# Optimization experiments

Hardware: AMD Instinct MI355X
Metric: run time of the kernel (lower is better)

Reference implementation:

```python
import jax, jax.numpy as jnp
import numpy as np

EPS = 1e-5

def _layernorm(x, g, b):
    mu = jnp.mean(x, axis=-1, keepdims=True)
    var = jnp.mean(jnp.square(x - mu), axis=-1, keepdims=True)
    return (x - mu) * jax.lax.rsqrt(var + EPS) * g + b

def setup_inputs() -> dict:
    key = jax.random.key(0)
    B, N, C, MID = 1, 512, 128, 128
    ks = jax.random.split(key, 12)
    s_c = 1.0 / np.sqrt(C)
    s_m = 1.0 / np.sqrt(MID)
    return {
        "act": jax.random.normal(ks[0], (B, N, N, C), dtype=jnp.float32),
        "mask": jnp.ones((B, N, N), dtype=jnp.float32),
        # input LayerNorm
        "ln_in_g": jnp.ones((C,), jnp.float32),
        "ln_in_b": jnp.zeros((C,), jnp.float32),
        # left/right projections and gates (Linear: y = x @ W + b)
        "wl": jax.random.normal(ks[1], (C, MID), jnp.float32) * s_c,
        "bl": jnp.zeros((MID,), jnp.float32),
        "wr": jax.random.normal(ks[2], (C, MID), jnp.float32) * s_c,
        "br": jnp.zeros((MID,), jnp.float32),
        "wgl": jax.random.normal(ks[3], (C, MID), jnp.float32) * s_c,
        "bgl": jnp.zeros((MID,), jnp.float32),
        "wgr": jax.random.normal(ks[4], (C, MID), jnp.float32) * s_c,
        "bgr": jnp.zeros((MID,), jnp.float32),
        # output gating linear (C -> C)
        "wgate": jax.random.normal(ks[5], (C, C), jnp.float32) * s_c,
        "bgate": jnp.zeros((C,), jnp.float32),
        # center LayerNorm (over MID)
        "ln_c_g": jnp.ones((MID,), jnp.float32),
        "ln_c_b": jnp.zeros((MID,), jnp.float32),
        # output projection (MID -> C)
        "wout": jax.random.normal(ks[6], (MID, C), jnp.float32) * s_m,
        "bout": jnp.zeros((C,), jnp.float32),
    }

def reference(act, mask, ln_in_g, ln_in_b, wl, bl, wr, br, wgl, bgl, wgr, bgr,
              wgate, bgate, ln_c_g, ln_c_b, wout, bout):
    x = _layernorm(act, ln_in_g, ln_in_b)          # [B,N,N,C]
    m = mask[..., None]                             # [B,N,N,1]
    left_proj = m * (x @ wl + bl) * jax.nn.sigmoid(x @ wgl + bgl)   # [B,N,N,MID]
    right_proj = m * (x @ wr + br) * jax.nn.sigmoid(x @ wgr + bgr)  # [B,N,N,MID]
    gate_values = x @ wgate + bgate                 # [B,N,N,C]
    # triangle outgoing: contract over k (second index of both)
    out = jnp.einsum('bikc,bjkc->bijc', left_proj, right_proj)      # [B,N,N,MID]
    out = _layernorm(out, ln_c_g, ln_c_b)
    out = out @ wout + bout                         # [B,N,N,C]
    return out * jax.nn.sigmoid(gate_values)
```

## Files before the change

kernel.cpp:

```cpp
#include <hip/hip_runtime.h>

#define NPOS 512
#define NN_ (512 * 512)

typedef unsigned short u16;
typedef __attribute__((ext_vector_type(8))) short bf16x8_t;
typedef __attribute__((ext_vector_type(4))) float f32x4_t;

__device__ __forceinline__ float bf2f(u16 u) {
  union { unsigned int i; float f; } v;
  v.i = ((unsigned int)u) << 16;
  return v.f;
}
__device__ __forceinline__ u16 f2bf(float f) {
  __bf16 h = (__bf16)f;
  return __builtin_bit_cast(unsigned short, h);
}
__device__ __forceinline__ float sigm(float x) { return 1.0f / (1.0f + __expf(-x)); }

__device__ __forceinline__ void gld_lds16(u16* lds, const u16* g) {
  __builtin_amdgcn_global_load_lds(
      (const __attribute__((address_space(1))) unsigned int*)g,
      (__attribute__((address_space(3))) unsigned int*)lds, 16, 0, 0);
}

__global__ __launch_bounds__(256) void k0_wt(const float* __restrict__ wl,
                                             const float* __restrict__ wgl,
                                             const float* __restrict__ wr,
                                             const float* __restrict__ wgr,
                                             const float* __restrict__ wgate,
                                             u16* __restrict__ wtbase) {
  int b = blockIdx.x;
  int wi = b >> 3;
  int o0 = (b & 7) * 16;
  const float* W = wi == 0 ? wl : wi == 1 ? wgl : wi == 2 ? wr : wi == 3 ? wgr : wgate;
  u16* dst = wtbase + wi * 16384;
  int t = threadIdx.x;
  int o = o0 + (t >> 4);
  int k0 = (t & 15) * 8;
  float v[8];
#pragma unroll
  for (int i = 0; i < 8; ++i) v[i] = W[(k0 + i) * 128 + o];
  ushort4 a, b4;
  a.x = f2bf(v[0]); a.y = f2bf(v[1]); a.z = f2bf(v[2]); a.w = f2bf(v[3]);
  b4.x = f2bf(v[4]); b4.y = f2bf(v[5]); b4.z = f2bf(v[6]); b4.w = f2bf(v[7]);
  *(ushort4*)(dst + o * 128 + k0) = a;
  *(ushort4*)(dst + o * 128 + k0 + 4) = b4;
}

__global__ __launch_bounds__(256) void k0b(const float* __restrict__ wout,
                                           u16* __restrict__ Wt6) {
  int o = blockIdx.x * 16 + (threadIdx.x >> 4);
  int k0 = (threadIdx.x & 15) * 8;
  float v[8];
#pragma unroll
  for (int i = 0; i < 8; ++i) v[i] = wout[(k0 + i) * 128 + o];
  ushort4 a, b4;
  a.x = f2bf(v[0]); a.y = f2bf(v[1]); a.z = f2bf(v[2]); a.w = f2bf(v[3]);
  b4.x = f2bf(v[4]); b4.y = f2bf(v[5]); b4.z = f2bf(v[6]); b4.w = f2bf(v[7]);
  *(ushort4*)(Wt6 + o * 128 + k0) = a;
  *(ushort4*)(Wt6 + o * 128 + k0 + 4) = b4;
}

__global__ __launch_bounds__(512, 4) void k2_fused(
    const float* __restrict__ act, const float* __restrict__ mask,
    const u16* __restrict__ wtbase,
    const float* __restrict__ ln_g, const float* __restrict__ ln_b,
    const float* __restrict__ bl, const float* __restrict__ bgl,
    const float* __restrict__ br, const float* __restrict__ bgr,
    const float* __restrict__ bgate,
    u16* __restrict__ Lt, u16* __restrict__ Rt, u16* __restrict__ Gs) {
  __shared__ __align__(16) unsigned char smem[81920];
  u16* xn  = (u16*)smem;
  u16* wh0 = (u16*)(smem + 32768);
  u16* wh1 = (u16*)(smem + 49152);
  u16* ob  = (u16*)(smem + 65536);

  int tid = threadIdx.x;
  int l = tid & 63, w = tid >> 6;
  int wr_ = w >> 1, wc = w & 1;
  int lr = l & 15, lk = l >> 4;
  size_t p0 = (size_t)blockIdx.x * 128;

#define STAGE(i_, buf_)                                                     \
  {                                                                         \
    const u16* src = wtbase + ((i_) >> 1) * 16384 + ((i_) & 1) * 8192;      \
    _Pragma("unroll") for (int q = 0; q < 2; ++q) {                         \
      int s = q * 512 + tid;                                                \
      int row = s >> 4, j = (s & 15) ^ (row & 7);                           \
      gld_lds16((buf_) + s * 8, src + row * 128 + j * 8);                   \
    }                                                                       \
  }
#define ZERO(ACC)                                                           \
  { ACC[0][0] = (f32x4_t){0.f, 0.f, 0.f, 0.f};                              \
    ACC[0][1] = (f32x4_t){0.f, 0.f, 0.f, 0.f};                              \
    ACC[1][0] = (f32x4_t){0.f, 0.f, 0.f, 0.f};                              \
    ACC[1][1] = (f32x4_t){0.f, 0.f, 0.f, 0.f}; }
#define MFK(buf_, ACC, KT, AF0, AF1)                                        \
  {                                                                         \
    int kb = (KT) * 4 + lk;                                                 \
    int o0_ = wc * 32 + lr, o1_ = wc * 32 + 16 + lr;                        \
    bf16x8_t bfr0 = *(const bf16x8_t*)((buf_) + o0_ * 128 + ((kb ^ (o0_ & 7)) * 8)); \
    bf16x8_t bfr1 = *(const bf16x8_t*)((buf_) + o1_ * 128 + ((kb ^ (o1_ & 7)) * 8)); \
    ACC[0][0] = __builtin_amdgcn_mfma_f32_16x16x32_bf16(AF0, bfr0, ACC[0][0], 0, 0, 0); \
    ACC[0][1] = __builtin_amdgcn_mfma_f32_16x16x32_bf16(AF0, bfr1, ACC[0][1], 0, 0, 0); \
    ACC[1][0] = __builtin_amdgcn_mfma_f32_16x16x32_bf16(AF1, bfr0, ACC[1][0], 0, 0, 0); \
    ACC[1][1] = __builtin_amdgcn_mfma_f32_16x16x32_bf16(AF1, bfr1, ACC[1][1], 0, 0, 0); \
  }
#define MF(buf_, ACC)                                                       \
  MFK(buf_, ACC, 0, af00, af10)                                             \
  MFK(buf_, ACC, 1, af01, af11)                                             \
  MFK(buf_, ACC, 2, af02, af12)                                             \
  MFK(buf_, ACC, 3, af03, af13)
#define MFPAIR(ACCP, ACCG)                                                  \
  __builtin_amdgcn_s_setprio(1);                                            \
  ZERO(ACCP); MF(wh0, ACCP);                                                \
  ZERO(ACCG); MF(wh1, ACCG);                                                \
  __builtin_amdgcn_s_setprio(0);
#define EPW(ACCP, ACCG, Bp_, Bg_, obase_)                                   \
  {                                                                         \
    float bpv[2], bgv[2];                                                   \
    _Pragma("unroll") for (int n = 0; n < 2; ++n) {                         \
      int og = (obase_) + wc * 32 + n * 16 + lr;                            \
      bpv[n] = Bp_[og]; bgv[n] = Bg_[og];                                   \
    }                                                                       \
    _Pragma("unroll") for (int m = 0; m < 2; ++m) {                         \
      int p4 = wr_ * 32 + m * 16 + lk * 4;                                  \
      float4 mk = *(const float4*)(mask + p0 + p4);                         \
      int slot = p4 >> 3, off = p4 & 7;                                     \
      _Pragma("unroll") for (int n = 0; n < 2; ++n) {                       \
        int ol = wc * 32 + n * 16 + lr;                                     \
        ushort4 v;                                                          \
        v.x = f2bf(mk.x * (ACCP[m][n][0] + bpv[n]) * sigm(ACCG[m][n][0] + bgv[n])); \
        v.y = f2bf(mk.y * (ACCP[m][n][1] + bpv[n]) * sigm(ACCG[m][n][1] + bgv[n])); \
        v.z = f2bf(mk.z * (ACCP[m][n][2] + bpv[n]) * sigm(ACCG[m][n][2] + bgv[n])); \
        v.w = f2bf(mk.w * (ACCP[m][n][3] + bpv[n]) * sigm(ACCG[m][n][3] + bgv[n])); \
        *(ushort4*)(ob + ol * 128 + ((slot ^ (ol & 7)) << 3) + off) = v;    \
      }                                                                     \
    }                                                                       \
  }
#define GEPW(ACC, obase_)                                                   \
  {                                                                         \
    float bgv[2];                                                           \
    _Pragma("unroll") for (int n = 0; n < 2; ++n)                           \
      bgv[n] = bgate[(obase_) + wc * 32 + n * 16 + lr];                     \
    _Pragma("unroll") for (int m = 0; m < 2; ++m) {                         \
      int p4 = wr_ * 32 + m * 16 + lk * 4;                                  \
      int slot = p4 >> 3, off = p4 & 7;                                     \
      _Pragma("unroll") for (int n = 0; n < 2; ++n) {                       \
        int ol = wc * 32 + n * 16 + lr;                                     \
        ushort4 v;                                                          \
        v.x = f2bf(ACC[m][n][0] + bgv[n]);                                  \
        v.y = f2bf(ACC[m][n][1] + bgv[n]);                                  \
        v.z = f2bf(ACC[m][n][2] + bgv[n]);                                  \
        v.w = f2bf(ACC[m][n][3] + bgv[n]);                                  \
        *(ushort4*)(ob + ol * 128 + ((slot ^ (ol & 7)) << 3) + off) = v;    \
      }                                                                     \
    }                                                                       \
  }
#define EPS(Tdst_, obase_)                                                  \
  {                                                                         \
    _Pragma("unroll") for (int it = 0; it < 2; ++it) {                      \
      int s = it * 512 + tid;                                               \
      int ol = s >> 4, c8 = s & 15;                                         \
      *(uint4*)(Tdst_ + (size_t)((obase_) + ol) * NN_ + p0 + c8 * 8) =      \
          *(const uint4*)(ob + ol * 128 + ((c8 ^ (ol & 7)) << 3));          \
    }                                                                       \
  }

  STAGE(0, wh0);
  STAGE(2, wh1);

#pragma unroll
  for (int r = 0; r < 8; ++r) {
    int f = r * 512 + tid;
    int pos = f >> 5, c4 = f & 31;
    float4 v = *(const float4*)(act + (p0 + pos) * 128 + c4 * 4);
    float s1 = v.x + v.y + v.z + v.w;
    float s2 = v.x * v.x + v.y * v.y + v.z * v.z + v.w * v.w;
#pragma unroll
    for (int m = 1; m < 32; m <<= 1) {
      s1 += __shfl_xor(s1, m);
      s2 += __shfl_xor(s2, m);
    }
    float mu = s1 * (1.0f / 128.0f);
    float rstd = rsqrtf(s2 * (1.0f / 128.0f) - mu * mu + 1e-5f);
    int cb = c4 * 4;
    float4 gg = *(const float4*)(ln_g + cb);
    float4 bb = *(const float4*)(ln_b + cb);
    ushort4 o4;
    o4.x = f2bf((v.x - mu) * rstd * gg.x + bb.x);
    o4.y = f2bf((v.y - mu) * rstd * gg.y + bb.y);
    o4.z = f2bf((v.z - mu) * rstd * gg.z + bb.z);
    o4.w = f2bf((v.w - mu) * rstd * gg.w + bb.w);
    int c8 = c4 >> 1, off = (c4 & 1) * 4;
    *(ushort4*)(xn + pos * 128 + ((c8 ^ (pos & 7)) << 3) + off) = o4;
  }
  __syncthreads();

  bf16x8_t af00, af01, af02, af03, af10, af11, af12, af13;
  {
    int row0 = wr_ * 32 + lr;
    int row1 = wr_ * 32 + 16 + lr;
    const u16* x0 = xn + row0 * 128;
    const u16* x1 = xn + row1 * 128;
    af00 = *(const bf16x8_t*)(x0 + (((0 * 4 + lk) ^ (row0 & 7)) * 8));
    af01 = *(const bf16x8_t*)(x0 + (((1 * 4 + lk) ^ (row0 & 7)) * 8));
    af02 = *(const bf16x8_t*)(x0 + (((2 * 4 + lk) ^ (row0 & 7)) * 8));
    af03 = *(const bf16x8_t*)(x0 + (((3 * 4 + lk) ^ (row0 & 7)) * 8));
    af10 = *(const bf16x8_t*)(x1 + (((0 * 4 + lk) ^ (row1 & 7)) * 8));
    af11 = *(const bf16x8_t*)(x1 + (((1 * 4 + lk) ^ (row1 & 7)) * 8));
    af12 = *(const bf16x8_t*)(x1 + (((2 * 4 + lk) ^ (row1 & 7)) * 8));
    af13 = *(const bf16x8_t*)(x1 + (((3 * 4 + lk) ^ (row1 & 7)) * 8));
  }

  f32x4_t ap[2][2], ag[2][2];

  MFPAIR(ap, ag);
  __syncthreads();
  STAGE(1, wh0);
  STAGE(3, wh1);
  EPW(ap, ag, bl, bgl, 0);
  __syncthreads();
  EPS(Lt, 0);

  MFPAIR(ap, ag);
  __syncthreads();
  STAGE(4, wh0);
  STAGE(6, wh1);
  EPW(ap, ag, bl, bgl, 64);
  __syncthreads();
  EPS(Lt, 64);

  MFPAIR(ap, ag);
  __syncthreads();
  STAGE(5, wh0);
  STAGE(7, wh1);
  EPW(ap, ag, br, bgr, 0);
  __syncthreads();
  EPS(Rt, 0);

  MFPAIR(ap, ag);
  __syncthreads();
  STAGE(8, wh0);
  STAGE(9, wh1);
  EPW(ap, ag, br, bgr, 64);
  __syncthreads();
  EPS(Rt, 64);

  MFPAIR(ap, ag);
  __syncthreads();
  GEPW(ap, 0);
  __syncthreads();
  EPS(Gs, 0);
  __syncthreads();
  GEPW(ag, 64);
  __syncthreads();
  EPS(Gs, 64);
#undef STAGE
#undef ZERO
#undef MFK
#undef MF
#undef MFPAIR
#undef EPW
#undef GEPW
#undef EPS
}

__global__ __launch_bounds__(256, 4) void k3_einsum_mfma(const u16* __restrict__ Lt,
                                                         const u16* __restrict__ Rt,
                                                         u16* __restrict__ Ot) {
  __shared__ __align__(16) u16 smem[2 * 128 * 64];
  u16* La = smem;
  u16* Rb = smem + 128 * 64;

  int tid = threadIdx.x;
  int bid = blockIdx.x;
  int swz = (bid & 7) * 256 + (bid >> 3);
  int c = swz >> 4;
  int t = swz & 15;
  int i0 = (t >> 2) << 7, j0 = (t & 3) << 7;
  const u16* Lg = Lt + (size_t)c * NN_ + (size_t)i0 * 512;
  const u16* Rg = Rt + (size_t)c * NN_ + (size_t)j0 * 512;

  int l = tid & 63, w = tid >> 6;
  int wr = w >> 1, wc = w & 1;
  int lr = l & 15, lk = l >> 4;

  f32x4_t acc[4][4];
#pragma unroll
  for (int m = 0; m < 4; ++m)
#pragma unroll
    for (int n = 0; n < 4; ++n) acc[m][n] = (f32x4_t){0.f, 0.f, 0.f, 0.f};

  for (int kt = 0; kt < 512; kt += 64) {
#pragma unroll
    for (int q = 0; q < 4; ++q) {
      int s = q * 256 + tid;
      int row = s >> 3;
      int k8 = (s & 7) ^ (row & 7);
      gld_lds16(La + s * 8, Lg + (size_t)row * 512 + kt + k8 * 8);
      gld_lds16(Rb + s * 8, Rg + (size_t)row * 512 + kt + k8 * 8);
    }
    __syncthreads();

    __builtin_amdgcn_s_setprio(1);
#pragma unroll
    for (int ks = 0; ks < 2; ++ks) {
      int kb = ks * 4 + lk;
      bf16x8_t af[4], bf[4];
#pragma unroll
      for (int m = 0; m < 4; ++m) {
        int row = wr * 64 + m * 16 + lr;
        af[m] = *(const bf16x8_t*)(La + row * 64 + ((kb ^ (row & 7)) * 8));
      }
#pragma unroll
      for (int n = 0; n < 4; ++n) {
        int row = wc * 64 + n * 16 + lr;
        bf[n] = *(const bf16x8_t*)(Rb + row * 64 + ((kb ^ (row & 7)) * 8));
      }
#pragma unroll
      for (int m = 0; m < 4; ++m)
#pragma unroll
        for (int n = 0; n < 4; ++n)
          acc[m][n] = __builtin_amdgcn_mfma_f32_16x16x32_bf16(af[m], bf[n], acc[m][n], 0, 0, 0);
    }
    __builtin_amdgcn_s_setprio(0);
    __syncthreads();
  }

  u16* ob = smem;
#pragma unroll
  for (int m = 0; m < 4; ++m) {
    int row0 = wr * 64 + m * 16 + lk * 4;
#pragma unroll
    for (int n = 0; n < 4; ++n) {
      int col = (wc * 64 + n * 16 + lr) ^ (lk << 4);
#pragma unroll
      for (int r = 0; r < 4; ++r)
        ob[(row0 + r) * 128 + col] = f2bf(acc[m][n][r]);
    }
  }
  __syncthreads();
#pragma unroll
  for (int it = 0; it < 8; ++it) {
    int s = it * 256 + tid;
    int row = s >> 4, c8 = s & 15;
    int g = (row >> 2) & 3;
    const u16* src = ob + row * 128 + ((c8 * 8) ^ (g << 4));
    *(uint4*)(Ot + (size_t)c * NN_ + (size_t)(i0 + row) * 512 + j0 + c8 * 8) =
        *(const uint4*)src;
  }
}

__global__ __launch_bounds__(512, 4) void k4_mfma(const u16* __restrict__ Ot,
                                                  const u16* __restrict__ Gs,
                                                  const u16* __restrict__ Wt6,
                                                  const float* __restrict__ gc,
                                                  const float* __restrict__ bc,
                                                  const float* __restrict__ bout,
                                                  float* __restrict__ out) {
  __shared__ __align__(16) unsigned char smem[70656];
  u16* ot = (u16*)smem;
  u16* ws = (u16*)(smem + 32768);
  float* ps = (float*)(smem + 65536);
  float* pss = (float*)(smem + 67584);
  float2* munr = (float2*)(smem + 69632);

  int tid = threadIdx.x;
  int l = tid & 63, w = tid >> 6;
  int wr = w >> 1, wc = w & 1;
  int lr = l & 15, lk = l >> 4;
  size_t p0 = (size_t)blockIdx.x * 128;
  int i_row = (int)(p0 >> 9);
  int j0 = (int)(p0 & 511);

#pragma unroll
  for (int q = 0; q < 4; ++q) {
    int s = q * 512 + tid;
    int cc = s >> 4, j = s & 15;
    gld_lds16(ot + s * 8, Ot + (size_t)cc * NN_ + (size_t)i_row * 512 + j0 + j * 8);
  }
#pragma unroll
  for (int q = 0; q < 4; ++q) {
    int s = q * 512 + tid;
    int o = s >> 4, j = (s & 15) ^ (o & 7);
    gld_lds16(ws + s * 8, Wt6 + o * 128 + j * 8);
  }
  __syncthreads();

  int g = tid >> 7, pos = tid & 127;
  float vals[32];
  float s1 = 0.0f, s2 = 0.0f;
#pragma unroll
  for (int m = 0; m < 32; ++m) {
    float v = bf2f(ot[(g * 32 + m) * 128 + pos]);
    vals[m] = v;
    s1 += v;
    s2 += v * v;
  }
  ps[g * 128 + pos] = s1;
  pss[g * 128 + pos] = s2;
  __syncthreads();
  if (tid < 128) {
    float a = ps[tid] + ps[128 + tid] + ps[256 + tid] + ps[384 + tid];
    float b = pss[tid] + pss[128 + tid] + pss[256 + tid] + pss[384 + tid];
    float mu = a * (1.0f / 128.0f);
    float rstd = rsqrtf(b * (1.0f / 128.0f) - mu * mu + 1e-5f);
    munr[tid] = make_float2(mu, rstd);
  }
  __syncthreads();
  float2 mr = munr[pos];

  u16* xn = ot;
#pragma unroll
  for (int mm = 0; mm < 4; ++mm) {
    int c8 = g * 4 + mm;
    ushort4 va, vb;
    int cb = c8 * 8;
    va.x = f2bf((vals[mm * 8 + 0] - mr.x) * mr.y * gc[cb + 0] + bc[cb + 0]);
    va.y = f2bf((vals[mm * 8 + 1] - mr.x) * mr.y * gc[cb + 1] + bc[cb + 1]);
    va.z = f2bf((vals[mm * 8 + 2] - mr.x) * mr.y * gc[cb + 2] + bc[cb + 2]);
    va.w = f2bf((vals[mm * 8 + 3] - mr.x) * mr.y * gc[cb + 3] + bc[cb + 3]);
    vb.x = f2bf((vals[mm * 8 + 4] - mr.x) * mr.y * gc[cb + 4] + bc[cb + 4]);
    vb.y = f2bf((vals[mm * 8 + 5] - mr.x) * mr.y * gc[cb + 5] + bc[cb + 5]);
    vb.z = f2bf((vals[mm * 8 + 6] - mr.x) * mr.y * gc[cb + 6] + bc[cb + 6]);
    vb.w = f2bf((vals[mm * 8 + 7] - mr.x) * mr.y * gc[cb + 7] + bc[cb + 7]);
    int slot = (c8 ^ (pos & 7)) * 8;
    *(ushort4*)(xn + pos * 128 + slot) = va;
    *(ushort4*)(xn + pos * 128 + slot + 4) = vb;
  }
  __syncthreads();

  f32x4_t acc[2][4];
#pragma unroll
  for (int m = 0; m < 2; ++m)
#pragma unroll
    for (int n = 0; n < 4; ++n) acc[m][n] = (f32x4_t){0.f, 0.f, 0.f, 0.f};

  __builtin_amdgcn_s_setprio(1);
#pragma unroll
  for (int kt = 0; kt < 4; ++kt) {
    int kb = kt * 4 + lk;
    bf16x8_t af[2], bf[4];
#pragma unroll
    for (int m = 0; m < 2; ++m) {
      int row = wr * 32 + m * 16 + lr;
      af[m] = *(const bf16x8_t*)(xn + row * 128 + ((kb ^ (row & 7)) * 8));
    }
#pragma unroll
    for (int n = 0; n < 4; ++n) {
      int o = wc * 64 + n * 16 + lr;
      bf[n] = *(const bf16x8_t*)(ws + o * 128 + ((kb ^ (o & 7)) * 8));
    }
#pragma unroll
    for (int m = 0; m < 2; ++m)
#pragma unroll
      for (int n = 0; n < 4; ++n)
        acc[m][n] = __builtin_amdgcn_mfma_f32_16x16x32_bf16(af[m], bf[n], acc[m][n], 0, 0, 0);
  }
  __builtin_amdgcn_s_setprio(0);

  float* os = (float*)(smem + 32768);
#pragma unroll
  for (int h = 0; h < 2; ++h) {
    __syncthreads();
    if ((wr >> 1) == h) {
      int rb = (wr & 1) * 32;
#pragma unroll
      for (int n = 0; n < 4; ++n) {
        int o = wc * 64 + n * 16 + lr;
        float bo = bout[o];
#pragma unroll
        for (int m = 0; m < 2; ++m) {
          int p = rb + m * 16 + lk * 4;
          ushort4 g4 = *(const ushort4*)(Gs + (size_t)o * NN_ + p0 + h * 64 + p);
          float gv[4] = {sigm(bf2f(g4.x)), sigm(bf2f(g4.y)),
                         sigm(bf2f(g4.z)), sigm(bf2f(g4.w))};
#pragma unroll
          for (int r = 0; r < 4; ++r) {
            int row = p + r;
            os[row * 128 + (o ^ (((row >> 2) & 7) << 4))] = (acc[m][n][r] + bo) * gv[r];
          }
        }
      }
    }
    __syncthreads();
#pragma unroll
    for (int it = 0; it < 4; ++it) {
      int s = it * 512 + tid;
      int row = s >> 5, sl = s & 31;
      float4 v = *(const float4*)(os + row * 128 + ((sl * 4) ^ (((row >> 2) & 7) << 4)));
      *(float4*)(out + (p0 + h * 64 + row) * 128 + sl * 4) = v;
    }
  }
}

extern "C" void kernel_launch(void* const* d_in, const int* in_sizes, int n_in,
                              void* d_out, int out_size, void* d_ws, size_t ws_size,
                              hipStream_t stream) {
  const float* act    = (const float*)d_in[0];
  const float* mask   = (const float*)d_in[1];
  const float* ln_in_g = (const float*)d_in[2];
  const float* ln_in_b = (const float*)d_in[3];
  const float* wl     = (const float*)d_in[4];
  const float* bl     = (const float*)d_in[5];
  const float* wr     = (const float*)d_in[6];
  const float* br     = (const float*)d_in[7];
  const float* wgl    = (const float*)d_in[8];
  const float* bgl    = (const float*)d_in[9];
  const float* wgr    = (const float*)d_in[10];
  const float* bgr    = (const float*)d_in[11];
  const float* wgate  = (const float*)d_in[12];
  const float* bgate  = (const float*)d_in[13];
  const float* ln_c_g = (const float*)d_in[14];
  const float* ln_c_b = (const float*)d_in[15];
  const float* wout   = (const float*)d_in[16];
  const float* bout   = (const float*)d_in[17];
  float* out = (float*)d_out;

  char* ws = (char*)d_ws;
  const size_t SEG = 1ull << 26;
  u16* Lt  = (u16*)(ws);
  u16* Rt  = (u16*)(ws + 1 * SEG);
  u16* Gs  = (u16*)(ws + 2 * SEG);
  u16* Ot  = (u16*)(ws + 3 * SEG);
  u16* Wt6 = Lt;

  u16* wtbase = (u16*)((char*)d_out + (size_t)out_size * 4 - 5 * 32768);

  k0_wt<<<dim3(40), dim3(256), 0, stream>>>(wl, wgl, wr, wgr, wgate, wtbase);
  k2_fused<<<dim3(2048), dim3(512), 0, stream>>>(act, mask, wtbase, ln_in_g, ln_in_b,
                                                 bl, bgl, br, bgr, bgate, Lt, Rt, Gs);
  k3_einsum_mfma<<<dim3(2048), dim3(256), 0, stream>>>(Lt, Rt, Ot);
  k0b<<<dim3(8), dim3(256), 0, stream>>>(wout, Wt6);
  k4_mfma<<<dim3(2048), dim3(512), 0, stream>>>(Ot, Gs, Wt6, ln_c_g, ln_c_b, bout, out);
}
```

Baseline: 258.3 us.

## Move gate projection from k2 into k4 by storing normalized input instead

Instead of computing the gate linear in the projection kernel and writing gate values in a channel-major layout, k2 now writes the bf16 layernormed input row-major and k4 recomputes the gate GEMM with MFMA before its epilogue. The aim is to shorten k2 and replace strided channel-major gate reads in k4 with a contiguous tile load into LDS. It adds a GEMM, an LDS load of the input and gate weights, and extra registers to k4. The bytes of the intermediate buffer stay the same.

```diff
diff --git a/kernel.cpp b/kernel.cpp
--- a/kernel.cpp
+++ b/kernel.cpp
@@ -68,8 +68,7 @@
     const float* __restrict__ ln_g, const float* __restrict__ ln_b,
     const float* __restrict__ bl, const float* __restrict__ bgl,
     const float* __restrict__ br, const float* __restrict__ bgr,
-    const float* __restrict__ bgate,
-    u16* __restrict__ Lt, u16* __restrict__ Rt, u16* __restrict__ Gs) {
+    u16* __restrict__ Lt, u16* __restrict__ Rt, u16* __restrict__ Gx) {
   __shared__ __align__(16) unsigned char smem[81920];
   u16* xn  = (u16*)smem;
   u16* wh0 = (u16*)(smem + 32768);
@@ -139,25 +138,6 @@
       }                                                                     \
     }                                                                       \
   }
-#define GEPW(ACC, obase_)                                                   \
-  {                                                                         \
-    float bgv[2];                                                           \
-    _Pragma("unroll") for (int n = 0; n < 2; ++n)                           \
-      bgv[n] = bgate[(obase_) + wc * 32 + n * 16 + lr];                     \
-    _Pragma("unroll") for (int m = 0; m < 2; ++m) {                         \
-      int p4 = wr_ * 32 + m * 16 + lk * 4;                                  \
-      int slot = p4 >> 3, off = p4 & 7;                                     \
-      _Pragma("unroll") for (int n = 0; n < 2; ++n) {                       \
-        int ol = wc * 32 + n * 16 + lr;                                     \
-        ushort4 v;                                                          \
-        v.x = f2bf(ACC[m][n][0] + bgv[n]);                                  \
-        v.y = f2bf(ACC[m][n][1] + bgv[n]);                                  \
-        v.z = f2bf(ACC[m][n][2] + bgv[n]);                                  \
-        v.w = f2bf(ACC[m][n][3] + bgv[n]);                                  \
-        *(ushort4*)(ob + ol * 128 + ((slot ^ (ol & 7)) << 3) + off) = v;    \
-      }                                                                     \
-    }                                                                       \
-  }
 #define EPS(Tdst_, obase_)                                                  \
   {                                                                         \
     _Pragma("unroll") for (int it = 0; it < 2; ++it) {                      \
@@ -214,6 +194,14 @@
     af13 = *(const bf16x8_t*)(x1 + (((3 * 4 + lk) ^ (row1 & 7)) * 8));
   }
 
+#pragma unroll
+  for (int q = 0; q < 4; ++q) {
+    int s = q * 512 + tid;
+    int row = s >> 4, c8 = s & 15;
+    *(uint4*)(Gx + (p0 + row) * 128 + c8 * 8) =
+        *(const uint4*)(xn + row * 128 + c8 * 8);
+  }
+
   f32x4_t ap[2][2], ag[2][2];
 
   MFPAIR(ap, ag);
@@ -242,28 +230,15 @@
 
   MFPAIR(ap, ag);
   __syncthreads();
-  STAGE(8, wh0);
-  STAGE(9, wh1);
   EPW(ap, ag, br, bgr, 64);
   __syncthreads();
   EPS(Rt, 64);
-
-  MFPAIR(ap, ag);
-  __syncthreads();
-  GEPW(ap, 0);
-  __syncthreads();
-  EPS(Gs, 0);
-  __syncthreads();
-  GEPW(ag, 64);
-  __syncthreads();
-  EPS(Gs, 64);
 #undef STAGE
 #undef ZERO
 #undef MFK
 #undef MF
 #undef MFPAIR
 #undef EPW
-#undef GEPW
 #undef EPS
 }
 
@@ -354,13 +329,17 @@
 }
 
 __global__ __launch_bounds__(512, 4) void k4_mfma(const u16* __restrict__ Ot,
-                                                  const u16* __restrict__ Gs,
+                                                  const u16* __restrict__ Gx,
+                                                  const u16* __restrict__ wtbase,
                                                   const u16* __restrict__ Wt6,
+                                                  const float* __restrict__ bgate,
                                                   const float* __restrict__ gc,
                                                   const float* __restrict__ bc,
                                                   const float* __restrict__ bout,
                                                   float* __restrict__ out) {
   __shared__ __align__(16) unsigned char smem[70656];
+  u16* xg = (u16*)smem;
+  u16* wg = (u16*)(smem + 32768);
   u16* ot = (u16*)smem;
   u16* ws = (u16*)(smem + 32768);
   float* ps = (float*)(smem + 65536);
@@ -374,6 +353,66 @@
   size_t p0 = (size_t)blockIdx.x * 128;
   int i_row = (int)(p0 >> 9);
   int j0 = (int)(p0 & 511);
+
+#pragma unroll
+  for (int q = 0; q < 4; ++q) {
+    int s = q * 512 + tid;
+    int row = s >> 4, c8 = s & 15;
+    gld_lds16(xg + s * 8, Gx + (p0 + row) * 128 + c8 * 8);
+  }
+  {
+    const u16* wsrc = wtbase + 4 * 16384;
+#pragma unroll
+    for (int q = 0; q < 4; ++q) {
+      int s = q * 512 + tid;
+      int row = s >> 4, j = (s & 15) ^ (row & 7);
+      gld_lds16(wg + s * 8, wsrc + row * 128 + j * 8);
+    }
+  }
+  __syncthreads();
+
+  f32x4_t gacc[2][4];
+#pragma unroll
+  for (int m = 0; m < 2; ++m)
+#pragma unroll
+    for (int n = 0; n < 4; ++n) gacc[m][n] = (f32x4_t){0.f, 0.f, 0.f, 0.f};
+
+  __builtin_amdgcn_s_setprio(1);
+#pragma unroll
+  for (int kt = 0; kt < 4; ++kt) {
+    int kb = kt * 4 + lk;
+    bf16x8_t af[2], bf[4];
+#pragma unroll
+    for (int m = 0; m < 2; ++m) {
+      int row = wr * 32 + m * 16 + lr;
+      af[m] = *(const bf16x8_t*)(xg + row * 128 + ((kb ^ (row & 7)) * 8));
+    }
+#pragma unroll
+    for (int n = 0; n < 4; ++n) {
+      int o = wc * 64 + n * 16 + lr;
+      bf[n] = *(const bf16x8_t*)(wg + o * 128 + ((kb ^ (o & 7)) * 8));
+    }
+#pragma unroll
+    for (int m = 0; m < 2; ++m)
+#pragma unroll
+      for (int n = 0; n < 4; ++n)
+        gacc[m][n] = __builtin_amdgcn_mfma_f32_16x16x32_bf16(af[m], bf[n], gacc[m][n], 0, 0, 0);
+  }
+  __builtin_amdgcn_s_setprio(0);
+
+  ushort4 gb[2][4];
+#pragma unroll
+  for (int n = 0; n < 4; ++n) {
+    float bg = bgate[wc * 64 + n * 16 + lr];
+#pragma unroll
+    for (int m = 0; m < 2; ++m) {
+      gb[m][n].x = f2bf(gacc[m][n][0] + bg);
+      gb[m][n].y = f2bf(gacc[m][n][1] + bg);
+      gb[m][n].z = f2bf(gacc[m][n][2] + bg);
+      gb[m][n].w = f2bf(gacc[m][n][3] + bg);
+    }
+  }
+  __syncthreads();
 
 #pragma unroll
   for (int q = 0; q < 4; ++q) {
@@ -466,17 +505,15 @@
   for (int h = 0; h < 2; ++h) {
     __syncthreads();
     if ((wr >> 1) == h) {
-      int rb = (wr & 1) * 32;
 #pragma unroll
       for (int n = 0; n < 4; ++n) {
         int o = wc * 64 + n * 16 + lr;
         float bo = bout[o];
 #pragma unroll
         for (int m = 0; m < 2; ++m) {
-          int p = rb + m * 16 + lk * 4;
-          ushort4 g4 = *(const ushort4*)(Gs + (size_t)o * NN_ + p0 + h * 64 + p);
-          float gv[4] = {sigm(bf2f(g4.x)), sigm(bf2f(g4.y)),
-                         sigm(bf2f(g4.z)), sigm(bf2f(g4.w))};
+          int p = (wr & 1) * 32 + m * 16 + lk * 4;
+          float gv[4] = {sigm(bf2f(gb[m][n].x)), sigm(bf2f(gb[m][n].y)),
+                         sigm(bf2f(gb[m][n].z)), sigm(bf2f(gb[m][n].w))};
 #pragma unroll
           for (int r = 0; r < 4; ++r) {
             int row = p + r;
@@ -523,7 +560,7 @@
   const size_t SEG = 1ull << 26;
   u16* Lt  = (u16*)(ws);
   u16* Rt  = (u16*)(ws + 1 * SEG);
-  u16* Gs  = (u16*)(ws + 2 * SEG);
+  u16* Gx  = (u16*)(ws + 2 * SEG);
   u16* Ot  = (u16*)(ws + 3 * SEG);
   u16* Wt6 = Lt;
 
@@ -531,8 +568,9 @@
 
   k0_wt<<<dim3(40), dim3(256), 0, stream>>>(wl, wgl, wr, wgr, wgate, wtbase);
   k2_fused<<<dim3(2048), dim3(512), 0, stream>>>(act, mask, wtbase, ln_in_g, ln_in_b,
-                                                 bl, bgl, br, bgr, bgate, Lt, Rt, Gs);
+                                                 bl, bgl, br, bgr, Lt, Rt, Gx);
   k3_einsum_mfma<<<dim3(2048), dim3(256), 0, stream>>>(Lt, Rt, Ot);
   k0b<<<dim3(8), dim3(256), 0, stream>>>(wout, Wt6);
-  k4_mfma<<<dim3(2048), dim3(512), 0, stream>>>(Ot, Gs, Wt6, ln_c_g, ln_c_b, bout, out);
-}
+  k4_mfma<<<dim3(2048), dim3(512), 0, stream>>>(Ot, Gx, wtbase, Wt6, bgate,
+                                                ln_c_g, ln_c_b, bout, out);
+}
```

Result: faster. 248.9 us (-3.6%).
